# Kernel tuning notes

Measured on AMD Instinct MI355X. Metric: run time of the kernel, lower is better.

Reference implementation:

```python
import jax, jax.numpy as jnp
import numpy as np

B, N, S = 8, 4096, 1024          # clouds, points per cloud, fps samples per cloud
C_IN = 64
R_LIST = (0.1, 0.2, 0.4)
K_LIST = (16, 32, 64)
CHANNELS = ([C_IN + 3, 64, 64, 128], [C_IN + 3, 128, 128, 256], [C_IN + 3, 128, 128, 256])


def setup_inputs() -> dict:
    key = jax.random.key(0)
    ks = jax.random.split(key, 2 + 9)
    inp = {}
    inp["x"] = jax.random.normal(ks[0], (B * N, C_IN), jnp.float32)
    inp["pos"] = jax.random.uniform(ks[1], (B * N, 3), jnp.float32)
    inp["batch"] = jnp.repeat(jnp.arange(B, dtype=jnp.int32), N)
    ki = 2
    for s, ch in enumerate(CHANNELS):
        for l in range(len(ch) - 1):
            inp[f"W{s}_{l}"] = jax.random.normal(ks[ki], (ch[l], ch[l + 1]), jnp.float32) / np.float32(np.sqrt(ch[l]))
            inp[f"b{s}_{l}"] = jnp.zeros((ch[l + 1],), jnp.float32)
        ki += 1
    return inp


def _fps_one(pos_b):
    """Farthest point sampling on one cloud [N,3] -> [S] int32 indices (start at 0)."""
    def step(carry, _):
        min_d, last = carry
        d = jnp.sum((pos_b - pos_b[last]) ** 2, axis=-1)          # [N]
        min_d = jnp.minimum(min_d, d)
        return (min_d, jnp.argmax(min_d).astype(jnp.int32)), last
    init = (jnp.full((N,), jnp.inf, pos_b.dtype), jnp.int32(0))
    _, idx = jax.lax.scan(step, init, None, length=S)
    return idx


def _scale(xb, posb, centers, r, K, Ws, bs):
    """Radius ball query (K nearest within r) + PointConv (MLP on [x_j, pos_j-pos_i], max-aggr)."""
    d2 = jnp.sum((centers[:, None, :] - posb[None, :, :]) ** 2, axis=-1)  # [S,N]
    neg = jnp.where(d2 <= r * r, -d2, -jnp.inf)
    vals, nbr = jax.lax.top_k(neg, K)                                      # [S,K]
    valid = vals > -jnp.inf                                                # center itself always valid
    feat = jnp.concatenate([xb[nbr], posb[nbr] - centers[:, None, :]], axis=-1)  # [S,K,C+3]
    h = feat
    for W, b in zip(Ws, bs):
        h = jax.nn.relu(h @ W + b)
    h = jnp.where(valid[..., None], h, -jnp.inf)
    return jnp.max(h, axis=1)                                              # [S,out]


def _forward(x, pos, batch, params):
    xb = x.reshape(B, N, C_IN)
    posb = pos.reshape(B, N, 3)
    idx = jax.vmap(_fps_one)(posb)                                # [B,S]
    centers = jnp.take_along_axis(posb, idx[..., None], axis=1)   # [B,S,3]
    outs = []
    for s in range(3):
        Ws, bs = params[s]
        f = lambda xb_, pb_, c_, Ws=Ws, bs=bs, s=s: _scale(xb_, pb_, c_, R_LIST[s], K_LIST[s], Ws, bs)
        outs.append(jax.vmap(f)(xb, posb, centers))
    new_x = jnp.concatenate(outs, axis=-1).reshape(B * S, -1)     # [B*S, 640]
    new_pos = centers.reshape(B * S, 3)
    new_batch = jnp.repeat(jnp.arange(B, dtype=batch.dtype), S)
    return new_x, new_pos, new_batch


def reference(x, pos, batch, W0_0, b0_0, W0_1, b0_1, W0_2, b0_2,
              W1_0, b1_0, W1_1, b1_1, W1_2, b1_2,
              W2_0, b2_0, W2_1, b2_1, W2_2, b2_2):
    params = (((W0_0, W0_1, W0_2), (b0_0, b0_1, b0_2)),
              ((W1_0, W1_1, W1_2), (b1_0, b1_1, b1_2)),
              ((W2_0, W2_1, W2_2), (b2_0, b2_1, b2_2)))
    return _forward(x, pos, batch, params)
```

## Files before the change

### kernel.cpp

```cpp
#include <hip/hip_runtime.h>

#define NB 8
#define NP 4096
#define NS 1024

typedef _Float16 f16x8 __attribute__((ext_vector_type(8)));
typedef _Float16 f16x4 __attribute__((ext_vector_type(4)));
typedef float f32x4 __attribute__((ext_vector_type(4)));

#define DPP_MAX(v, ctrl)                                                     \
    v = fmaxf(v, __int_as_float(__builtin_amdgcn_update_dpp(                 \
                __float_as_int(v), __float_as_int(v), (ctrl), 0xf, 0xf, false)))

__global__ __launch_bounds__(512, 1) void fps_kernel(
        const float* __restrict__ pos,
        float* __restrict__ centers,
        float* __restrict__ out_pos,
        float* __restrict__ out_batch) {
#pragma clang fp contract(off)
    const int b = blockIdx.x;
    const int tid = threadIdx.x;
    const int lane = tid & 63;
    const int wid = tid >> 6;
    __shared__ float4 slot[2][8];

    const float* pb = pos + (size_t)b * NP * 3;
    float px[8], py[8], pz[8], md[8];
    {
        const float4* pv = (const float4*)(pb + tid * 24);
        float4 q0 = pv[0], q1 = pv[1], q2 = pv[2];
        float4 q3 = pv[3], q4 = pv[4], q5 = pv[5];
        px[0] = q0.x; py[0] = q0.y; pz[0] = q0.z;
        px[1] = q0.w; py[1] = q1.x; pz[1] = q1.y;
        px[2] = q1.z; py[2] = q1.w; pz[2] = q2.x;
        px[3] = q2.y; py[3] = q2.z; pz[3] = q2.w;
        px[4] = q3.x; py[4] = q3.y; pz[4] = q3.z;
        px[5] = q3.w; py[5] = q4.x; pz[5] = q4.y;
        px[6] = q4.z; py[6] = q4.w; pz[6] = q5.x;
        px[7] = q5.y; py[7] = q5.z; pz[7] = q5.w;
    }
#pragma unroll
    for (int j = 0; j < 8; ++j) md[j] = __builtin_inff();
    for (int t = tid; t < NS; t += 512) out_batch[b * NS + t] = (float)b;

    float cx = pb[0], cy = pb[1], cz = pb[2];
    if (tid == 0) {
        size_t o = (size_t)(b * NS) * 3;
        centers[o + 0] = cx; centers[o + 1] = cy; centers[o + 2] = cz;
        out_pos[o + 0] = cx; out_pos[o + 1] = cy; out_pos[o + 2] = cz;
    }

    int par = 0;
    for (int t = 1; t < NS; ++t) {
        float bv = -1.0f, bx = cx, by = cy, bz = cz;
#pragma unroll
        for (int j = 0; j < 8; ++j) {
            float dx = px[j] - cx; float sx = dx * dx;
            float dy = py[j] - cy; float sy = dy * dy;
            float dz = pz[j] - cz; float sz = dz * dz;
            float d = sx + sy; d = d + sz;
            float m = fminf(md[j], d);
            md[j] = m;
            bool c = m > bv;
            bv = c ? m : bv;
            bx = c ? px[j] : bx;
            by = c ? py[j] : by;
            bz = c ? pz[j] : bz;
        }
        float v = bv;
        DPP_MAX(v, 0x111);
        DPP_MAX(v, 0x112);
        DPP_MAX(v, 0x114);
        DPP_MAX(v, 0x118);
        DPP_MAX(v, 0x142);
        DPP_MAX(v, 0x143);
        const float mx = __int_as_float(
            __builtin_amdgcn_readlane(__float_as_int(v), 63));
        unsigned long long tie = __ballot(bv == mx);
        if (lane == __ffsll(tie) - 1)
            slot[par][wid] = make_float4(mx, bx, by, bz);
        __syncthreads();
        float4 s0 = slot[par][0], s1 = slot[par][1];
        float4 s2 = slot[par][2], s3 = slot[par][3];
        float4 s4 = slot[par][4], s5 = slot[par][5];
        float4 s6 = slot[par][6], s7 = slot[par][7];
        float4 a01 = (s1.x > s0.x) ? s1 : s0;
        float4 a23 = (s3.x > s2.x) ? s3 : s2;
        float4 a45 = (s5.x > s4.x) ? s5 : s4;
        float4 a67 = (s7.x > s6.x) ? s7 : s6;
        float4 b03 = (a23.x > a01.x) ? a23 : a01;
        float4 b47 = (a67.x > a45.x) ? a67 : a45;
        float4 wn = (b47.x > b03.x) ? b47 : b03;
        cx = wn.y; cy = wn.z; cz = wn.w;
        if (tid == 0) {
            size_t o = (size_t)(b * NS + t) * 3;
            centers[o + 0] = cx; centers[o + 1] = cy; centers[o + 2] = cz;
            out_pos[o + 0] = cx; out_pos[o + 1] = cy; out_pos[o + 2] = cz;
        }
        par ^= 1;
    }
}

template <int K>
__device__ __forceinline__ void select_center(
        const float* __restrict__ pb,
        const float* __restrict__ centers,
        int* __restrict__ nbr, int* __restrict__ nvalid,
        float r2, int scid) {
#pragma clang fp contract(off)
    const int lane = threadIdx.x & 63;
    const unsigned kr2 = __float_as_uint(r2);
    const float cx = centers[scid * 3 + 0];
    const float cy = centers[scid * 3 + 1];
    const float cz = centers[scid * 3 + 2];

    unsigned key[64];
#pragma unroll
    for (int i = 0; i < 64; ++i) {
        const float* pp = pb + (size_t)(lane + i * 64) * 3;
        float dx = pp[0] - cx; float sx = dx * dx;
        float dy = pp[1] - cy; float sy = dy * dy;
        float dz = pp[2] - cz; float sz = dz * dz;
        float d2 = sx + sy; d2 = d2 + sz;
        key[i] = __float_as_uint(d2);
    }

    const unsigned long long below = (1ull << lane) - 1ull;
    int c_cnt = 0;
#pragma unroll
    for (int i = 0; i < 64; ++i)
        c_cnt += __popcll(__ballot(key[i] <= kr2));

    unsigned thr = kr2;
    int nv = c_cnt;
    bool need_ties = false;
    unsigned tkey = 0;
    if (c_cnt > K) {
        nv = K;
        unsigned lo = 0, hi = kr2;
        need_ties = true;
        while (lo < hi) {
            unsigned mid = lo + ((hi - lo) >> 1);
            int cnt = 0;
#pragma unroll
            for (int i = 0; i < 64; ++i)
                cnt += __popcll(__ballot(key[i] <= mid));
            if (cnt == K) { thr = mid; need_ties = false; break; }
            if (cnt > K) hi = mid; else lo = mid + 1;
        }
        tkey = lo;
    }

    if (!need_ties) {
        int base = 0;
#pragma unroll
        for (int i = 0; i < 64; ++i) {
            unsigned long long m = __ballot(key[i] <= thr);
            if (key[i] <= thr)
                nbr[(size_t)scid * K + base + __popcll(m & below)] = lane + i * 64;
            base += __popcll(m);
        }
    } else {
        const unsigned t = tkey;
        int m_cnt = 0;
#pragma unroll
        for (int i = 0; i < 64; ++i)
            m_cnt += __popcll(__ballot(key[i] < t));
        const int rem = K - m_cnt;
        int base = 0, tcnt = 0;
#pragma unroll
        for (int i = 0; i < 64; ++i) {
            unsigned long long lt = __ballot(key[i] < t);
            unsigned long long eq = __ballot(key[i] == t);
            if (key[i] < t) {
                nbr[(size_t)scid * K + base + __popcll(lt & below)] = lane + i * 64;
            } else if (key[i] == t) {
                int tr = tcnt + __popcll(eq & below);
                if (tr < rem) nbr[(size_t)scid * K + (m_cnt + tr)] = lane + i * 64;
            }
            base += __popcll(lt);
            tcnt += __popcll(eq);
        }
    }
    if (lane == 0) nvalid[scid] = nv;
}

__global__ __launch_bounds__(256) void select_all(
        const float* __restrict__ pos,
        const float* __restrict__ centers,
        int* __restrict__ nbr0, int* __restrict__ nbr1, int* __restrict__ nbr2,
        int* __restrict__ nvalid) {
    const int blk = blockIdx.x;
    const int seg = blk % 3;
    const int sblk = blk / 3;
    const int w = threadIdx.x >> 6;
    const int scid = sblk * 4 + w;
    const int b = scid >> 10;
    const float* pb = pos + (size_t)b * NP * 3;
    if (seg == 0)
        select_center<16>(pb, centers, nbr0, nvalid,
                          (float)(0.1 * 0.1), scid);
    else if (seg == 1)
        select_center<32>(pb, centers, nbr1, nvalid + 8192,
                          (float)(0.2 * 0.2), scid);
    else
        select_center<64>(pb, centers, nbr2, nvalid + 16384,
                          (float)(0.4 * 0.4), scid);
}

struct PrepArgs {
    const float* src[9];
    _Float16* dst[9];
    int kr[9], kp[9], nc[9];
};

__global__ __launch_bounds__(256) void prep_all(PrepArgs a) {
    const int m = blockIdx.y;
    const int kp = a.kp[m], kr = a.kr[m], nc = a.nc[m];
    const float* src = a.src[m];
    _Float16* dst = a.dst[m];
    const int tot = kp * nc;
    for (int i = blockIdx.x * 256 + threadIdx.x; i < tot; i += gridDim.x * 256) {
        int n = i / kp, k = i - n * kp;
        dst[i] = (k < kr) ? (_Float16)src[(size_t)k * nc + n] : (_Float16)0.f;
    }
}

template <int M, int C1, int C2, int C3, int OFF, int NCTR>
__device__ void mlp_body(
        char* smem,
        const float* __restrict__ x, const float* __restrict__ pos,
        const float* __restrict__ centers,
        const int* __restrict__ nbr, const int* __restrict__ nvalid,
        const _Float16* __restrict__ wt1, const _Float16* __restrict__ wt2,
        const _Float16* __restrict__ wt3,
        const float* __restrict__ b1, const float* __restrict__ b2,
        const float* __restrict__ b3,
        float* __restrict__ out, int blk) {
    constexpr int K1P = 96;
    constexpr int S1 = K1P + 8;
    constexpr int S2 = C1 + 8;
    constexpr int S3 = C2 + 8;
    constexpr int MT = M / 16;
    constexpr int NCH1 = C1 / 4, NCH2 = C2 / 4, NCH3 = C3 / 4;
    constexpr int NT1 = NCH1 / 16, NT2 = NCH2 / 16, NT3 = NCH3 / 16;
    constexpr int KT1 = K1P / 32, KT2 = C1 / 32, KT3 = C2 / 32;

    _Float16* feat = (_Float16*)smem;
    _Float16* h1 = feat + M * S1;
    _Float16* h2 = h1 + M * S2;
    int* outmax = (int*)(h2 + M * S3);

    const int tid = threadIdx.x;
    const int lane = tid & 63;
    const int w = tid >> 6;
    const int lm = lane & 15;
    const int lq = lane >> 4;

    f16x8 wf1[NT1][KT1], wf2[NT2][KT2], wf3[NT3][KT3];
    float bb1[NT1], bb2[NT2], bb3[NT3];
#pragma unroll
    for (int nt = 0; nt < NT1; ++nt) {
        int n = w * NCH1 + nt * 16 + lm;
        bb1[nt] = b1[n];
#pragma unroll
        for (int kt = 0; kt < KT1; ++kt)
            wf1[nt][kt] = *(const f16x8*)(wt1 + (size_t)n * K1P + kt * 32 + lq * 8);
    }
#pragma unroll
    for (int nt = 0; nt < NT2; ++nt) {
        int n = w * NCH2 + nt * 16 + lm;
        bb2[nt] = b2[n];
#pragma unroll
        for (int kt = 0; kt < KT2; ++kt)
            wf2[nt][kt] = *(const f16x8*)(wt2 + (size_t)n * C1 + kt * 32 + lq * 8);
    }
#pragma unroll
    for (int nt = 0; nt < NT3; ++nt) {
        int n = w * NCH3 + nt * 16 + lm;
        bb3[nt] = b3[n];
#pragma unroll
        for (int kt = 0; kt < KT3; ++kt)
            wf3[nt][kt] = *(const f16x8*)(wt3 + (size_t)n * C2 + kt * 32 + lq * 8);
    }

    for (int cc = 0; cc < NCTR; ++cc) {
        const int cid = blk * NCTR + cc;
        const int bidx = cid >> 10;
        const int nv = nvalid[cid];
        const float cx = centers[cid * 3 + 0];
        const float cy = centers[cid * 3 + 1];
        const float cz = centers[cid * 3 + 2];
        for (int i = tid; i < C3; i += 256) outmax[i] = 0;

#pragma unroll
        for (int it = tid; it < M * 16; it += 256) {
            const int r = it >> 4, sub = it & 15;
            if (r < nv) {
                int pt = nbr[(size_t)cid * M + r];
                float4 v = *(const float4*)(x + ((size_t)(bidx * NP) + pt) * 64 + sub * 4);
                f16x4 hv = {(_Float16)v.x, (_Float16)v.y, (_Float16)v.z, (_Float16)v.w};
                *(f16x4*)(feat + r * S1 + sub * 4) = hv;
            }
        }
#pragma unroll
        for (int it = tid; it < M * 4; it += 256) {
            const int r = it >> 2, q = it & 3;
            f16x8 z = {(_Float16)0.f, (_Float16)0.f, (_Float16)0.f, (_Float16)0.f,
                       (_Float16)0.f, (_Float16)0.f, (_Float16)0.f, (_Float16)0.f};
            if (q == 0 && r < nv) {
                int pt = nbr[(size_t)cid * M + r];
                const float* pr = pos + ((size_t)(bidx * NP) + pt) * 3;
                z[0] = (_Float16)(pr[0] - cx);
                z[1] = (_Float16)(pr[1] - cy);
                z[2] = (_Float16)(pr[2] - cz);
            }
            *(f16x8*)(feat + r * S1 + 64 + q * 8) = z;
        }
        __syncthreads();

#pragma unroll
        for (int mt = 0; mt < MT; ++mt) {
            f16x8 a[KT1];
#pragma unroll
            for (int kt = 0; kt < KT1; ++kt)
                a[kt] = *(const f16x8*)(feat + (mt * 16 + lm) * S1 + kt * 32 + lq * 8);
#pragma unroll
            for (int nt = 0; nt < NT1; ++nt) {
                f32x4 acc = {bb1[nt], bb1[nt], bb1[nt], bb1[nt]};
#pragma unroll
                for (int kt = 0; kt < KT1; ++kt)
                    acc = __builtin_amdgcn_mfma_f32_16x16x32_f16(a[kt], wf1[nt][kt], acc, 0, 0, 0);
                const int gc = w * NCH1 + nt * 16 + lm;
#pragma unroll
                for (int rg = 0; rg < 4; ++rg)
                    h1[(mt * 16 + lq * 4 + rg) * S2 + gc] = (_Float16)fmaxf(acc[rg], 0.f);
            }
        }
        __syncthreads();

#pragma unroll
        for (int mt = 0; mt < MT; ++mt) {
            f16x8 a[KT2];
#pragma unroll
            for (int kt = 0; kt < KT2; ++kt)
                a[kt] = *(const f16x8*)(h1 + (mt * 16 + lm) * S2 + kt * 32 + lq * 8);
#pragma unroll
            for (int nt = 0; nt < NT2; ++nt) {
                f32x4 acc = {bb2[nt], bb2[nt], bb2[nt], bb2[nt]};
#pragma unroll
                for (int kt = 0; kt < KT2; ++kt)
                    acc = __builtin_amdgcn_mfma_f32_16x16x32_f16(a[kt], wf2[nt][kt], acc, 0, 0, 0);
                const int gc = w * NCH2 + nt * 16 + lm;
#pragma unroll
                for (int rg = 0; rg < 4; ++rg)
                    h2[(mt * 16 + lq * 4 + rg) * S3 + gc] = (_Float16)fmaxf(acc[rg], 0.f);
            }
        }
        __syncthreads();

#pragma unroll
        for (int mt = 0; mt < MT; ++mt) {
            f16x8 a[KT3];
#pragma unroll
            for (int kt = 0; kt < KT3; ++kt)
                a[kt] = *(const f16x8*)(h2 + (mt * 16 + lm) * S3 + kt * 32 + lq * 8);
#pragma unroll
            for (int nt = 0; nt < NT3; ++nt) {
                f32x4 acc = {bb3[nt], bb3[nt], bb3[nt], bb3[nt]};
#pragma unroll
                for (int kt = 0; kt < KT3; ++kt)
                    acc = __builtin_amdgcn_mfma_f32_16x16x32_f16(a[kt], wf3[nt][kt], acc, 0, 0, 0);
                float mx = -1.f;
#pragma unroll
                for (int rg = 0; rg < 4; ++rg) {
                    int row = mt * 16 + lq * 4 + rg;
                    float v = fmaxf(acc[rg], 0.f);
                    if (row < nv) mx = fmaxf(mx, v);
                }
                mx = fmaxf(mx, __shfl_xor(mx, 16));
                mx = fmaxf(mx, __shfl_xor(mx, 32));
                if (lane < 16)
                    atomicMax(&outmax[w * NCH3 + nt * 16 + lm], __float_as_int(mx));
            }
        }
        __syncthreads();
        for (int i = tid; i < C3; i += 256)
            out[(size_t)cid * 640 + OFF + i] = __int_as_float(outmax[i]);
        __syncthreads();
    }
}

struct MlpW {
    const _Float16* w[9];
    const float* bias[9];
};

__global__ __launch_bounds__(256, 2) void mlp_all(
        const float* __restrict__ x, const float* __restrict__ pos,
        const float* __restrict__ centers,
        const int* __restrict__ nbr0, const int* __restrict__ nbr1,
        const int* __restrict__ nbr2, const int* __restrict__ nval,
        MlpW ww, float* __restrict__ out) {
    extern __shared__ char smem[];
    const int blk = blockIdx.x;
    if (blk < 1024)
        mlp_body<16, 64, 64, 128, 0, 8>(smem, x, pos, centers, nbr0, nval,
            ww.w[0], ww.w[1], ww.w[2], ww.bias[0], ww.bias[1], ww.bias[2], out, blk);
    else if (blk < 2048)
        mlp_body<32, 128, 128, 256, 128, 8>(smem, x, pos, centers, nbr1, nval + 8192,
            ww.w[3], ww.w[4], ww.w[5], ww.bias[3], ww.bias[4], ww.bias[5], out, blk - 1024);
    else
        mlp_body<64, 128, 128, 256, 384, 8>(smem, x, pos, centers, nbr2, nval + 16384,
            ww.w[6], ww.w[7], ww.w[8], ww.bias[6], ww.bias[7], ww.bias[8], out, blk - 2048);
}

extern "C" void kernel_launch(void* const* d_in, const int* in_sizes, int n_in,
                              void* d_out, int out_size, void* d_ws, size_t ws_size,
                              hipStream_t stream) {
    const float* x = (const float*)d_in[0];
    const float* pos = (const float*)d_in[1];
    const float* W0_0 = (const float*)d_in[3];
    const float* b0_0 = (const float*)d_in[4];
    const float* W0_1 = (const float*)d_in[5];
    const float* b0_1 = (const float*)d_in[6];
    const float* W0_2 = (const float*)d_in[7];
    const float* b0_2 = (const float*)d_in[8];
    const float* W1_0 = (const float*)d_in[9];
    const float* b1_0 = (const float*)d_in[10];
    const float* W1_1 = (const float*)d_in[11];
    const float* b1_1 = (const float*)d_in[12];
    const float* W1_2 = (const float*)d_in[13];
    const float* b1_2 = (const float*)d_in[14];
    const float* W2_0 = (const float*)d_in[15];
    const float* b2_0 = (const float*)d_in[16];
    const float* W2_1 = (const float*)d_in[17];
    const float* b2_1 = (const float*)d_in[18];
    const float* W2_2 = (const float*)d_in[19];
    const float* b2_2 = (const float*)d_in[20];

    float* out = (float*)d_out;
    char* ws = (char*)d_ws;
    float* centers = (float*)(ws + 0);
    int* nbr0 = (int*)(ws + 98304);
    int* nbr1 = (int*)(ws + 622592);
    int* nbr2 = (int*)(ws + 1671168);
    int* nval = (int*)(ws + 3768320);
    _Float16* w0t1 = (_Float16*)(ws + 3866624);
    _Float16* w0t2 = (_Float16*)(ws + 3878912);
    _Float16* w0t3 = (_Float16*)(ws + 3887104);
    _Float16* w1t1 = (_Float16*)(ws + 3903488);
    _Float16* w1t2 = (_Float16*)(ws + 3928064);
    _Float16* w1t3 = (_Float16*)(ws + 3960832);
    _Float16* w2t1 = (_Float16*)(ws + 4026368);
    _Float16* w2t2 = (_Float16*)(ws + 4050944);
    _Float16* w2t3 = (_Float16*)(ws + 4083712);

    float* out_pos = out + (size_t)8192 * 640;
    float* out_batch = out_pos + (size_t)8192 * 3;

    fps_kernel<<<dim3(NB), dim3(512), 0, stream>>>(pos, centers, out_pos, out_batch);

    select_all<<<dim3(6144), dim3(256), 0, stream>>>(pos, centers, nbr0, nbr1, nbr2, nval);

    PrepArgs pa;
    pa.src[0] = W0_0; pa.dst[0] = w0t1; pa.kr[0] = 67;  pa.kp[0] = 96;  pa.nc[0] = 64;
    pa.src[1] = W0_1; pa.dst[1] = w0t2; pa.kr[1] = 64;  pa.kp[1] = 64;  pa.nc[1] = 64;
    pa.src[2] = W0_2; pa.dst[2] = w0t3; pa.kr[2] = 64;  pa.kp[2] = 64;  pa.nc[2] = 128;
    pa.src[3] = W1_0; pa.dst[3] = w1t1; pa.kr[3] = 67;  pa.kp[3] = 96;  pa.nc[3] = 128;
    pa.src[4] = W1_1; pa.dst[4] = w1t2; pa.kr[4] = 128; pa.kp[4] = 128; pa.nc[4] = 128;
    pa.src[5] = W1_2; pa.dst[5] = w1t3; pa.kr[5] = 128; pa.kp[5] = 128; pa.nc[5] = 256;
    pa.src[6] = W2_0; pa.dst[6] = w2t1; pa.kr[6] = 67;  pa.kp[6] = 96;  pa.nc[6] = 128;
    pa.src[7] = W2_1; pa.dst[7] = w2t2; pa.kr[7] = 128; pa.kp[7] = 128; pa.nc[7] = 128;
    pa.src[8] = W2_2; pa.dst[8] = w2t3; pa.kr[8] = 128; pa.kp[8] = 128; pa.nc[8] = 256;
    prep_all<<<dim3(64, 9), dim3(256), 0, stream>>>(pa);

    MlpW ww;
    ww.w[0] = w0t1; ww.w[1] = w0t2; ww.w[2] = w0t3;
    ww.w[3] = w1t1; ww.w[4] = w1t2; ww.w[5] = w1t3;
    ww.w[6] = w2t1; ww.w[7] = w2t2; ww.w[8] = w2t3;
    ww.bias[0] = b0_0; ww.bias[1] = b0_1; ww.bias[2] = b0_2;
    ww.bias[3] = b1_0; ww.bias[4] = b1_1; ww.bias[5] = b1_2;
    ww.bias[6] = b2_0; ww.bias[7] = b2_1; ww.bias[8] = b2_2;

    mlp_all<<<dim3(3072), dim3(256), 49152, stream>>>(
        x, pos, centers, nbr0, nbr1, nbr2, nval, ww, out);
}
```

Measured before the change: 1.198 ms.

## Fuse FPS and ball-query into one persistent kernel with progress flags

Merges the farthest-point-sampling kernel and the neighbour-selection kernel into one launch. Eight blocks run FPS and publish progress counters every 16 centers with release stores. The remaining 248 blocks spin on those counters and run ball queries for centers as they become available. The aim is to hide the serial FPS latency behind the selection work. The scheme relies on all 256 blocks being co-resident, and it adds spin-wait overhead plus a memset launch.

```diff
diff --git a/kernel.cpp b/kernel.cpp
--- a/kernel.cpp
+++ b/kernel.cpp
@@ -11,95 +11,6 @@
 #define DPP_MAX(v, ctrl)                                                     \
     v = fmaxf(v, __int_as_float(__builtin_amdgcn_update_dpp(                 \
                 __float_as_int(v), __float_as_int(v), (ctrl), 0xf, 0xf, false)))
-
-__global__ __launch_bounds__(512, 1) void fps_kernel(
-        const float* __restrict__ pos,
-        float* __restrict__ centers,
-        float* __restrict__ out_pos,
-        float* __restrict__ out_batch) {
-#pragma clang fp contract(off)
-    const int b = blockIdx.x;
-    const int tid = threadIdx.x;
-    const int lane = tid & 63;
-    const int wid = tid >> 6;
-    __shared__ float4 slot[2][8];
-
-    const float* pb = pos + (size_t)b * NP * 3;
-    float px[8], py[8], pz[8], md[8];
-    {
-        const float4* pv = (const float4*)(pb + tid * 24);
-        float4 q0 = pv[0], q1 = pv[1], q2 = pv[2];
-        float4 q3 = pv[3], q4 = pv[4], q5 = pv[5];
-        px[0] = q0.x; py[0] = q0.y; pz[0] = q0.z;
-        px[1] = q0.w; py[1] = q1.x; pz[1] = q1.y;
-        px[2] = q1.z; py[2] = q1.w; pz[2] = q2.x;
-        px[3] = q2.y; py[3] = q2.z; pz[3] = q2.w;
-        px[4] = q3.x; py[4] = q3.y; pz[4] = q3.z;
-        px[5] = q3.w; py[5] = q4.x; pz[5] = q4.y;
-        px[6] = q4.z; py[6] = q4.w; pz[6] = q5.x;
-        px[7] = q5.y; py[7] = q5.z; pz[7] = q5.w;
-    }
-#pragma unroll
-    for (int j = 0; j < 8; ++j) md[j] = __builtin_inff();
-    for (int t = tid; t < NS; t += 512) out_batch[b * NS + t] = (float)b;
-
-    float cx = pb[0], cy = pb[1], cz = pb[2];
-    if (tid == 0) {
-        size_t o = (size_t)(b * NS) * 3;
-        centers[o + 0] = cx; centers[o + 1] = cy; centers[o + 2] = cz;
-        out_pos[o + 0] = cx; out_pos[o + 1] = cy; out_pos[o + 2] = cz;
-    }
-
-    int par = 0;
-    for (int t = 1; t < NS; ++t) {
-        float bv = -1.0f, bx = cx, by = cy, bz = cz;
-#pragma unroll
-        for (int j = 0; j < 8; ++j) {
-            float dx = px[j] - cx; float sx = dx * dx;
-            float dy = py[j] - cy; float sy = dy * dy;
-            float dz = pz[j] - cz; float sz = dz * dz;
-            float d = sx + sy; d = d + sz;
-            float m = fminf(md[j], d);
-            md[j] = m;
-            bool c = m > bv;
-            bv = c ? m : bv;
-            bx = c ? px[j] : bx;
-            by = c ? py[j] : by;
-            bz = c ? pz[j] : bz;
-        }
-        float v = bv;
-        DPP_MAX(v, 0x111);
-        DPP_MAX(v, 0x112);
-        DPP_MAX(v, 0x114);
-        DPP_MAX(v, 0x118);
-        DPP_MAX(v, 0x142);
-        DPP_MAX(v, 0x143);
-        const float mx = __int_as_float(
-            __builtin_amdgcn_readlane(__float_as_int(v), 63));
-        unsigned long long tie = __ballot(bv == mx);
-        if (lane == __ffsll(tie) - 1)
-            slot[par][wid] = make_float4(mx, bx, by, bz);
-        __syncthreads();
-        float4 s0 = slot[par][0], s1 = slot[par][1];
-        float4 s2 = slot[par][2], s3 = slot[par][3];
-        float4 s4 = slot[par][4], s5 = slot[par][5];
-        float4 s6 = slot[par][6], s7 = slot[par][7];
-        float4 a01 = (s1.x > s0.x) ? s1 : s0;
-        float4 a23 = (s3.x > s2.x) ? s3 : s2;
-        float4 a45 = (s5.x > s4.x) ? s5 : s4;
-        float4 a67 = (s7.x > s6.x) ? s7 : s6;
-        float4 b03 = (a23.x > a01.x) ? a23 : a01;
-        float4 b47 = (a67.x > a45.x) ? a67 : a45;
-        float4 wn = (b47.x > b03.x) ? b47 : b03;
-        cx = wn.y; cy = wn.z; cz = wn.w;
-        if (tid == 0) {
-            size_t o = (size_t)(b * NS + t) * 3;
-            centers[o + 0] = cx; centers[o + 1] = cy; centers[o + 2] = cz;
-            out_pos[o + 0] = cx; out_pos[o + 1] = cy; out_pos[o + 2] = cz;
-        }
-        par ^= 1;
-    }
-}
 
 template <int K>
 __device__ __forceinline__ void select_center(
@@ -185,27 +96,128 @@
     if (lane == 0) nvalid[scid] = nv;
 }
 
-__global__ __launch_bounds__(256) void select_all(
+__global__ __launch_bounds__(512, 1) void fps_select_fused(
         const float* __restrict__ pos,
-        const float* __restrict__ centers,
+        float* __restrict__ centers,
+        float* __restrict__ out_pos,
+        float* __restrict__ out_batch,
         int* __restrict__ nbr0, int* __restrict__ nbr1, int* __restrict__ nbr2,
-        int* __restrict__ nvalid) {
-    const int blk = blockIdx.x;
-    const int seg = blk % 3;
-    const int sblk = blk / 3;
-    const int w = threadIdx.x >> 6;
-    const int scid = sblk * 4 + w;
-    const int b = scid >> 10;
-    const float* pb = pos + (size_t)b * NP * 3;
-    if (seg == 0)
-        select_center<16>(pb, centers, nbr0, nvalid,
-                          (float)(0.1 * 0.1), scid);
-    else if (seg == 1)
-        select_center<32>(pb, centers, nbr1, nvalid + 8192,
-                          (float)(0.2 * 0.2), scid);
-    else
-        select_center<64>(pb, centers, nbr2, nvalid + 16384,
-                          (float)(0.4 * 0.4), scid);
+        int* __restrict__ nval,
+        unsigned* __restrict__ prog) {
+#pragma clang fp contract(off)
+    const int tid = threadIdx.x;
+    const int lane = tid & 63;
+
+    if (blockIdx.x < NB) {
+        const int b = blockIdx.x;
+        const int wid = tid >> 6;
+        __shared__ float4 slot[2][8];
+
+        const float* pb = pos + (size_t)b * NP * 3;
+        float px[8], py[8], pz[8], md[8];
+        {
+            const float4* pv = (const float4*)(pb + tid * 24);
+            float4 q0 = pv[0], q1 = pv[1], q2 = pv[2];
+            float4 q3 = pv[3], q4 = pv[4], q5 = pv[5];
+            px[0] = q0.x; py[0] = q0.y; pz[0] = q0.z;
+            px[1] = q0.w; py[1] = q1.x; pz[1] = q1.y;
+            px[2] = q1.z; py[2] = q1.w; pz[2] = q2.x;
+            px[3] = q2.y; py[3] = q2.z; pz[3] = q2.w;
+            px[4] = q3.x; py[4] = q3.y; pz[4] = q3.z;
+            px[5] = q3.w; py[5] = q4.x; pz[5] = q4.y;
+            px[6] = q4.z; py[6] = q4.w; pz[6] = q5.x;
+            px[7] = q5.y; py[7] = q5.z; pz[7] = q5.w;
+        }
+#pragma unroll
+        for (int j = 0; j < 8; ++j) md[j] = __builtin_inff();
+        for (int t = tid; t < NS; t += 512) out_batch[b * NS + t] = (float)b;
+
+        float cx = pb[0], cy = pb[1], cz = pb[2];
+        if (tid == 0) {
+            size_t o = (size_t)(b * NS) * 3;
+            centers[o + 0] = cx; centers[o + 1] = cy; centers[o + 2] = cz;
+            out_pos[o + 0] = cx; out_pos[o + 1] = cy; out_pos[o + 2] = cz;
+        }
+
+        int par = 0;
+        for (int t = 1; t < NS; ++t) {
+            float bv = -1.0f, bx = cx, by = cy, bz = cz;
+#pragma unroll
+            for (int j = 0; j < 8; ++j) {
+                float dx = px[j] - cx; float sx = dx * dx;
+                float dy = py[j] - cy; float sy = dy * dy;
+                float dz = pz[j] - cz; float sz = dz * dz;
+                float d = sx + sy; d = d + sz;
+                float m = fminf(md[j], d);
+                md[j] = m;
+                bool c = m > bv;
+                bv = c ? m : bv;
+                bx = c ? px[j] : bx;
+                by = c ? py[j] : by;
+                bz = c ? pz[j] : bz;
+            }
+            float v = bv;
+            DPP_MAX(v, 0x111);
+            DPP_MAX(v, 0x112);
+            DPP_MAX(v, 0x114);
+            DPP_MAX(v, 0x118);
+            DPP_MAX(v, 0x142);
+            DPP_MAX(v, 0x143);
+            const float mx = __int_as_float(
+                __builtin_amdgcn_readlane(__float_as_int(v), 63));
+            unsigned long long tie = __ballot(bv == mx);
+            if (lane == __ffsll(tie) - 1)
+                slot[par][wid] = make_float4(mx, bx, by, bz);
+            __syncthreads();
+            float4 s0 = slot[par][0], s1 = slot[par][1];
+            float4 s2 = slot[par][2], s3 = slot[par][3];
+            float4 s4 = slot[par][4], s5 = slot[par][5];
+            float4 s6 = slot[par][6], s7 = slot[par][7];
+            float4 a01 = (s1.x > s0.x) ? s1 : s0;
+            float4 a23 = (s3.x > s2.x) ? s3 : s2;
+            float4 a45 = (s5.x > s4.x) ? s5 : s4;
+            float4 a67 = (s7.x > s6.x) ? s7 : s6;
+            float4 b03 = (a23.x > a01.x) ? a23 : a01;
+            float4 b47 = (a67.x > a45.x) ? a67 : a45;
+            float4 wn = (b47.x > b03.x) ? b47 : b03;
+            cx = wn.y; cy = wn.z; cz = wn.w;
+            if (tid == 0) {
+                size_t o = (size_t)(b * NS + t) * 3;
+                centers[o + 0] = cx; centers[o + 1] = cy; centers[o + 2] = cz;
+                out_pos[o + 0] = cx; out_pos[o + 1] = cy; out_pos[o + 2] = cz;
+                if ((t & 15) == 15)
+                    __hip_atomic_store(&prog[b], (unsigned)(t + 1),
+                                       __ATOMIC_RELEASE, __HIP_MEMORY_SCOPE_AGENT);
+            }
+            par ^= 1;
+        }
+    } else {
+        const int wblk = blockIdx.x - NB;
+        const int wid = tid >> 6;
+        const int wave_id = wblk * 8 + wid;
+        const int NWAVE = 248 * 8;
+        const int NTASK = 3 * NB * NS;
+        for (int T = wave_id; T < NTASK; T += NWAVE) {
+            const int s = T / 24;
+            const int r = T - s * 24;
+            const int b = r & 7;
+            const int seg = r >> 3;
+            const int scid = b * NS + s;
+            while (__hip_atomic_load(&prog[b], __ATOMIC_ACQUIRE,
+                                     __HIP_MEMORY_SCOPE_AGENT) <= (unsigned)s)
+                __builtin_amdgcn_s_sleep(4);
+            const float* pb = pos + (size_t)b * NP * 3;
+            if (seg == 0)
+                select_center<16>(pb, centers, nbr0, nval,
+                                  (float)(0.1 * 0.1), scid);
+            else if (seg == 1)
+                select_center<32>(pb, centers, nbr1, nval + 8192,
+                                  (float)(0.2 * 0.2), scid);
+            else
+                select_center<64>(pb, centers, nbr2, nval + 16384,
+                                  (float)(0.4 * 0.4), scid);
+        }
+    }
 }
 
 struct PrepArgs {
@@ -455,13 +467,15 @@
     _Float16* w2t1 = (_Float16*)(ws + 4026368);
     _Float16* w2t2 = (_Float16*)(ws + 4050944);
     _Float16* w2t3 = (_Float16*)(ws + 4083712);
+    unsigned* prog = (unsigned*)(ws + 4149248);
 
     float* out_pos = out + (size_t)8192 * 640;
     float* out_batch = out_pos + (size_t)8192 * 3;
 
-    fps_kernel<<<dim3(NB), dim3(512), 0, stream>>>(pos, centers, out_pos, out_batch);
-
-    select_all<<<dim3(6144), dim3(256), 0, stream>>>(pos, centers, nbr0, nbr1, nbr2, nval);
+    hipMemsetAsync(prog, 0, NB * sizeof(unsigned), stream);
+
+    fps_select_fused<<<dim3(256), dim3(512), 0, stream>>>(
+        pos, centers, out_pos, out_batch, nbr0, nbr1, nbr2, nval, prog);
 
     PrepArgs pa;
     pa.src[0] = W0_0; pa.dst[0] = w0t1; pa.kr[0] = 67;  pa.kp[0] = 96;  pa.nc[0] = 64;
```

Result: faster. 1.116 ms (-6.8%).
